# Performance work log

Measured on AMD Instinct MI355X. Metric: run time of the kernel, lower is better.

## Reference

```python
import jax, jax.numpy as jnp
import numpy as np

HIDDEN = 128
HEADS = 8
HEAD_DIM = HIDDEN // HEADS


def setup_inputs() -> dict:
    key = jax.random.key(0)
    ks = jax.random.split(key, 10)
    B, V = 2, 768
    s = 1.0 / np.sqrt(HIDDEN)
    return {
        "x": jax.random.normal(ks[0], (B, V, HIDDEN), dtype=jnp.float32),
        "edge_gate": jax.random.uniform(ks[1], (B, V, V, HIDDEN), dtype=jnp.float32),
        "Wq": jax.random.normal(ks[2], (HIDDEN, HIDDEN), dtype=jnp.float32) * s,
        "bq": jnp.zeros((HIDDEN,), dtype=jnp.float32),
        "Wk": jax.random.normal(ks[3], (HIDDEN, HIDDEN), dtype=jnp.float32) * s,
        "bk": jnp.zeros((HIDDEN,), dtype=jnp.float32),
        "Wv": jax.random.normal(ks[4], (HIDDEN, HIDDEN), dtype=jnp.float32) * s,
        "bv": jnp.zeros((HIDDEN,), dtype=jnp.float32),
        "Wo": jax.random.normal(ks[5], (HIDDEN, HIDDEN), dtype=jnp.float32) * s,
        "bo": jnp.zeros((HIDDEN,), dtype=jnp.float32),
    }


def reference(x, edge_gate, Wq, bq, Wk, bk, Wv, bv, Wo, bo):
    B, V, H = x.shape
    nh, hd = HEADS, HEAD_DIM
    # torch Linear: y = x @ W.T + b
    q = (x @ Wq.T + bq).reshape(B, V, nh, hd).transpose(0, 2, 1, 3)  # (B,nh,V,hd)
    k = (x @ Wk.T + bk).reshape(B, V, nh, hd).transpose(0, 2, 1, 3)
    v = (x @ Wv.T + bv).reshape(B, V, nh, hd).transpose(0, 2, 1, 3)
    scores = jnp.einsum("bhqd,bhkd->bhqk", q, k) / jnp.sqrt(jnp.float32(hd))
    edge_mask = jnp.mean(edge_gate, axis=-1)[:, None]  # (B,1,V,V)
    weights = jax.nn.softmax(scores * edge_mask, axis=-1)
    attended = jnp.einsum("bhqk,bhkd->bhqd", weights, v)
    attended = attended.transpose(0, 2, 1, 3).reshape(B, V, H)
    return attended @ Wo.T + bo
```

## Files before the change

kernel.cpp:

```cpp
#include <hip/hip_runtime.h>
#include <math.h>

#define BB 2
#define VV 768
#define HID 128
#define NH 8
#define HD 16

#define QKV_BLOCKS 768
#define EDGE_BLOCKS 2048
#define EDGE_WAVES (EDGE_BLOCKS * 4)
#define NPAIR (BB * VV * VV / 2)
#define EDGE_ITERS (NPAIR / EDGE_WAVES)

__global__ __launch_bounds__(256) void fused_qkv_edgemean(
    const float* __restrict__ x, const float* __restrict__ eg,
    const float* __restrict__ Wq, const float* __restrict__ bq,
    const float* __restrict__ Wk, const float* __restrict__ bk,
    const float* __restrict__ Wv, const float* __restrict__ bv,
    float* __restrict__ qh, float* __restrict__ kh, float* __restrict__ vh,
    float* __restrict__ mask) {
    __shared__ float xs[2][HID];
    if (blockIdx.x < QKV_BLOCKS) {
        const int half = threadIdx.x >> 7;
        const int c    = threadIdx.x & 127;
        const int row  = blockIdx.x * 2 + half;
        xs[half][c] = x[row * HID + c];
        __syncthreads();
        const float4* xs4 = (const float4*)xs[half];
        const float4* wq4 = (const float4*)(Wq + c * HID);
        const float4* wk4 = (const float4*)(Wk + c * HID);
        const float4* wv4 = (const float4*)(Wv + c * HID);
        float aq = 0.f, ak = 0.f, av = 0.f;
#pragma unroll
        for (int k4 = 0; k4 < HID / 4; ++k4) {
            float4 xv = xs4[k4];
            float4 a = wq4[k4];
            aq += xv.x * a.x + xv.y * a.y + xv.z * a.z + xv.w * a.w;
            float4 bv2 = wk4[k4];
            ak += xv.x * bv2.x + xv.y * bv2.y + xv.z * bv2.z + xv.w * bv2.w;
            float4 cv = wv4[k4];
            av += xv.x * cv.x + xv.y * cv.y + xv.z * cv.z + xv.w * cv.w;
        }
        const int b = row / VV, vi = row - b * VV;
        const int idx = ((b * NH + (c >> 4)) * VV + vi) * HD + (c & 15);
        qh[idx] = aq + bq[c];
        kh[idx] = ak + bk[c];
        vh[idx] = av + bv[c];
    } else {
        const int l = threadIdx.x & 63;
        const int w = (blockIdx.x - QKV_BLOCKS) * 4 + (threadIdx.x >> 6);
        const float4* eg4 = (const float4*)eg;
        const size_t wbase = (size_t)w * (EDGE_ITERS * 64);
#pragma unroll 4
        for (int it = 0; it < EDGE_ITERS; ++it) {
            float4 v = eg4[wbase + it * 64 + l];
            float s = (v.x + v.y) + (v.z + v.w);
            s += __shfl_xor(s, 1);
            s += __shfl_xor(s, 2);
            s += __shfl_xor(s, 4);
            s += __shfl_xor(s, 8);
            s += __shfl_xor(s, 16);
            if ((l & 31) == 0) {
                const int p = w * EDGE_ITERS + it;
                mask[p * 2 + (l >> 5)] = s * (1.0f / 128.0f);
            }
        }
    }
}

__global__ __launch_bounds__(256) void attn_kernel(
    const float* __restrict__ qh, const float* __restrict__ kh,
    const float* __restrict__ vh, const float* __restrict__ mask,
    float* __restrict__ att) {
    __shared__ float sc[4][2][VV];
    const int wid  = threadIdx.x >> 6;
    const int lane = threadIdx.x & 63;
    const int gw   = blockIdx.x * 4 + wid;
    const int pr   = gw % (VV / 2);
    const int bh   = gw / (VV / 2);
    const int b    = bh >> 3, h = bh & 7;
    const int q0i  = pr * 2, q1i = q0i + 1;

    const float4* qp0 = (const float4*)(qh + ((size_t)bh * VV + q0i) * HD);
    const float4 qa0 = qp0[0], qa1 = qp0[1], qa2 = qp0[2], qa3 = qp0[3];
    const float4* qp1 = (const float4*)(qh + ((size_t)bh * VV + q1i) * HD);
    const float4 qb0 = qp1[0], qb1 = qp1[1], qb2 = qp1[2], qb3 = qp1[3];

    const float* mrow0 = mask + ((size_t)b * VV + q0i) * VV;
    const float* mrow1 = mrow0 + VV;
    const float* kbase = kh + (size_t)bh * VV * HD;
    const float* vbase = vh + (size_t)bh * VV * HD;

    float m0 = -INFINITY, m1 = -INFINITY;
#pragma unroll
    for (int t = 0; t < VV / 64; ++t) {
        const int j = lane + 64 * t;
        const float4* kp = (const float4*)(kbase + j * HD);
        float4 k0 = kp[0], k1 = kp[1], k2 = kp[2], k3 = kp[3];
        float d0 = qa0.x * k0.x + qa0.y * k0.y + qa0.z * k0.z + qa0.w * k0.w
                 + qa1.x * k1.x + qa1.y * k1.y + qa1.z * k1.z + qa1.w * k1.w
                 + qa2.x * k2.x + qa2.y * k2.y + qa2.z * k2.z + qa2.w * k2.w
                 + qa3.x * k3.x + qa3.y * k3.y + qa3.z * k3.z + qa3.w * k3.w;
        float d1 = qb0.x * k0.x + qb0.y * k0.y + qb0.z * k0.z + qb0.w * k0.w
                 + qb1.x * k1.x + qb1.y * k1.y + qb1.z * k1.z + qb1.w * k1.w
                 + qb2.x * k2.x + qb2.y * k2.y + qb2.z * k2.z + qb2.w * k2.w
                 + qb3.x * k3.x + qb3.y * k3.y + qb3.z * k3.z + qb3.w * k3.w;
        float s0 = d0 * 0.25f * mrow0[j];
        float s1 = d1 * 0.25f * mrow1[j];
        sc[wid][0][j] = s0;
        sc[wid][1][j] = s1;
        m0 = fmaxf(m0, s0);
        m1 = fmaxf(m1, s1);
    }
#pragma unroll
    for (int off = 1; off < 64; off <<= 1) {
        m0 = fmaxf(m0, __shfl_xor(m0, off));
        m1 = fmaxf(m1, __shfl_xor(m1, off));
    }

    float sum0 = 0.f, sum1 = 0.f;
    float acc0[HD], acc1[HD];
#pragma unroll
    for (int d = 0; d < HD; ++d) { acc0[d] = 0.f; acc1[d] = 0.f; }
#pragma unroll
    for (int t = 0; t < VV / 64; ++t) {
        const int j = lane + 64 * t;
        float e0 = __expf(sc[wid][0][j] - m0);
        float e1 = __expf(sc[wid][1][j] - m1);
        sum0 += e0;
        sum1 += e1;
        const float4* vp = (const float4*)(vbase + j * HD);
        float4 v0 = vp[0], v1 = vp[1], v2 = vp[2], v3 = vp[3];
        acc0[0]  += e0 * v0.x; acc0[1]  += e0 * v0.y; acc0[2]  += e0 * v0.z; acc0[3]  += e0 * v0.w;
        acc0[4]  += e0 * v1.x; acc0[5]  += e0 * v1.y; acc0[6]  += e0 * v1.z; acc0[7]  += e0 * v1.w;
        acc0[8]  += e0 * v2.x; acc0[9]  += e0 * v2.y; acc0[10] += e0 * v2.z; acc0[11] += e0 * v2.w;
        acc0[12] += e0 * v3.x; acc0[13] += e0 * v3.y; acc0[14] += e0 * v3.z; acc0[15] += e0 * v3.w;
        acc1[0]  += e1 * v0.x; acc1[1]  += e1 * v0.y; acc1[2]  += e1 * v0.z; acc1[3]  += e1 * v0.w;
        acc1[4]  += e1 * v1.x; acc1[5]  += e1 * v1.y; acc1[6]  += e1 * v1.z; acc1[7]  += e1 * v1.w;
        acc1[8]  += e1 * v2.x; acc1[9]  += e1 * v2.y; acc1[10] += e1 * v2.z; acc1[11] += e1 * v2.w;
        acc1[12] += e1 * v3.x; acc1[13] += e1 * v3.y; acc1[14] += e1 * v3.z; acc1[15] += e1 * v3.w;
    }
#pragma unroll
    for (int off = 1; off < 64; off <<= 1) {
        sum0 += __shfl_xor(sum0, off);
        sum1 += __shfl_xor(sum1, off);
    }

#pragma unroll
    for (int i = 0; i < 8; ++i) {
        float sa = (lane & 1) ? acc0[i] : acc0[i + 8];
        float ra = __shfl_xor(sa, 1);
        acc0[i] = ((lane & 1) ? acc0[i + 8] : acc0[i]) + ra;
        float sb = (lane & 1) ? acc1[i] : acc1[i + 8];
        float rb = __shfl_xor(sb, 1);
        acc1[i] = ((lane & 1) ? acc1[i + 8] : acc1[i]) + rb;
    }
#pragma unroll
    for (int i = 0; i < 4; ++i) {
        float sa = (lane & 2) ? acc0[i] : acc0[i + 4];
        float ra = __shfl_xor(sa, 2);
        acc0[i] = ((lane & 2) ? acc0[i + 4] : acc0[i]) + ra;
        float sb = (lane & 2) ? acc1[i] : acc1[i + 4];
        float rb = __shfl_xor(sb, 2);
        acc1[i] = ((lane & 2) ? acc1[i + 4] : acc1[i]) + rb;
    }
#pragma unroll
    for (int i = 0; i < 2; ++i) {
        float sa = (lane & 4) ? acc0[i] : acc0[i + 2];
        float ra = __shfl_xor(sa, 4);
        acc0[i] = ((lane & 4) ? acc0[i + 2] : acc0[i]) + ra;
        float sb = (lane & 4) ? acc1[i] : acc1[i + 2];
        float rb = __shfl_xor(sb, 4);
        acc1[i] = ((lane & 4) ? acc1[i + 2] : acc1[i]) + rb;
    }
    {
        float sa = (lane & 8) ? acc0[0] : acc0[1];
        float ra = __shfl_xor(sa, 8);
        acc0[0] = ((lane & 8) ? acc0[1] : acc0[0]) + ra;
        float sb = (lane & 8) ? acc1[0] : acc1[1];
        float rb = __shfl_xor(sb, 8);
        acc1[0] = ((lane & 8) ? acc1[1] : acc1[0]) + rb;
    }
    acc0[0] += __shfl_xor(acc0[0], 16);
    acc0[0] += __shfl_xor(acc0[0], 32);
    acc1[0] += __shfl_xor(acc1[0], 16);
    acc1[0] += __shfl_xor(acc1[0], 32);

    const int d = ((lane & 1) << 3) | ((lane & 2) << 1) | ((lane & 4) >> 1) | ((lane & 8) >> 3);
    if (lane < HD) {
        att[((size_t)b * VV + q0i) * HID + h * HD + d] = acc0[0] / sum0;
        att[((size_t)b * VV + q1i) * HID + h * HD + d] = acc1[0] / sum1;
    }
}

__global__ __launch_bounds__(128) void outproj_kernel(
    const float* __restrict__ att, const float* __restrict__ Wo,
    const float* __restrict__ bo, float* __restrict__ out) {
    const int row = blockIdx.x;
    const int c   = threadIdx.x;
    __shared__ float xs[HID];
    xs[c] = att[row * HID + c];
    __syncthreads();
    const float4* xs4 = (const float4*)xs;
    const float4* wo4 = (const float4*)(Wo + c * HID);
    float a = 0.f;
#pragma unroll
    for (int k4 = 0; k4 < HID / 4; ++k4) {
        float4 xv = xs4[k4];
        float4 wv = wo4[k4];
        a += xv.x * wv.x + xv.y * wv.y + xv.z * wv.z + xv.w * wv.w;
    }
    out[row * HID + c] = a + bo[c];
}

extern "C" void kernel_launch(void* const* d_in, const int* in_sizes, int n_in,
                              void* d_out, int out_size, void* d_ws, size_t ws_size,
                              hipStream_t stream) {
    const float* x  = (const float*)d_in[0];
    const float* eg = (const float*)d_in[1];
    const float* Wq = (const float*)d_in[2];
    const float* bq = (const float*)d_in[3];
    const float* Wk = (const float*)d_in[4];
    const float* bk = (const float*)d_in[5];
    const float* Wv = (const float*)d_in[6];
    const float* bv = (const float*)d_in[7];
    const float* Wo = (const float*)d_in[8];
    const float* bo = (const float*)d_in[9];
    float* out = (float*)d_out;

    float* ws   = (float*)d_ws;
    float* mask = ws;
    float* qh   = mask + (size_t)BB * VV * VV;
    float* kh   = qh + (size_t)BB * VV * HID;
    float* vh   = kh + (size_t)BB * VV * HID;
    float* att  = vh + (size_t)BB * VV * HID;

    hipLaunchKernelGGL(fused_qkv_edgemean, dim3(QKV_BLOCKS + EDGE_BLOCKS), dim3(256), 0, stream,
                       x, eg, Wq, bq, Wk, bk, Wv, bv, qh, kh, vh, mask);
    hipLaunchKernelGGL(attn_kernel, dim3(BB * NH * VV / 8), dim3(256), 0, stream,
                       qh, kh, vh, mask, att);
    hipLaunchKernelGGL(outproj_kernel, dim3(BB * VV), dim3(128), 0, stream,
                       att, Wo, bo, out);
}
```

Baseline: 219.3 us.

## Reduce edge-gate rows per thread instead of wave-cooperative shuffle reduction

The edge-mean pass changes from wave-cooperative coalesced float4 loads with shuffle reductions to one thread per pair of rows. Each thread sums 256 contiguous floats in registers and writes one float2. The grid becomes one block per 512 rows, and edge blocks are placed ahead of the QKV blocks. This removes the shuffles and the strided scalar stores, but each load instruction now hits 64 addresses 1 KB apart, which risks poor coalescing and cache-line thrashing on the dominant 600 MB stream.

Result: slower. 227.4 us (+3.7%).

```diff
diff --git a/kernel.cpp b/kernel.cpp
--- a/kernel.cpp
+++ b/kernel.cpp
@@ -7,11 +7,9 @@
 #define NH 8
 #define HD 16
 
+#define NROWS (BB * VV * VV)
+#define EDGE_BLOCKS (NROWS / 2 / 256)
 #define QKV_BLOCKS 768
-#define EDGE_BLOCKS 2048
-#define EDGE_WAVES (EDGE_BLOCKS * 4)
-#define NPAIR (BB * VV * VV / 2)
-#define EDGE_ITERS (NPAIR / EDGE_WAVES)
 
 __global__ __launch_bounds__(256) void fused_qkv_edgemean(
     const float* __restrict__ x, const float* __restrict__ eg,
@@ -21,10 +19,32 @@
     float* __restrict__ qh, float* __restrict__ kh, float* __restrict__ vh,
     float* __restrict__ mask) {
     __shared__ float xs[2][HID];
-    if (blockIdx.x < QKV_BLOCKS) {
+    if (blockIdx.x < EDGE_BLOCKS) {
+        const int g = blockIdx.x * 256 + threadIdx.x;
+        const float4* p = (const float4*)eg + (size_t)g * 64;
+        float a0x = 0.f, a0y = 0.f, a0z = 0.f, a0w = 0.f;
+        float a1x = 0.f, a1y = 0.f, a1z = 0.f, a1w = 0.f;
+#pragma unroll
+        for (int kg = 0; kg < 8; ++kg) {
+#pragma unroll
+            for (int k4 = 0; k4 < 4; ++k4) {
+                float4 v = p[kg * 4 + k4];
+                a0x += v.x; a0y += v.y; a0z += v.z; a0w += v.w;
+            }
+#pragma unroll
+            for (int k4 = 0; k4 < 4; ++k4) {
+                float4 v = p[32 + kg * 4 + k4];
+                a1x += v.x; a1y += v.y; a1z += v.z; a1w += v.w;
+            }
+        }
+        float2 st;
+        st.x = ((a0x + a0y) + (a0z + a0w)) * (1.0f / 128.0f);
+        st.y = ((a1x + a1y) + (a1z + a1w)) * (1.0f / 128.0f);
+        ((float2*)mask)[g] = st;
+    } else {
         const int half = threadIdx.x >> 7;
         const int c    = threadIdx.x & 127;
-        const int row  = blockIdx.x * 2 + half;
+        const int row  = (blockIdx.x - EDGE_BLOCKS) * 2 + half;
         xs[half][c] = x[row * HID + c];
         __syncthreads();
         const float4* xs4 = (const float4*)xs[half];
@@ -47,25 +67,6 @@
         qh[idx] = aq + bq[c];
         kh[idx] = ak + bk[c];
         vh[idx] = av + bv[c];
-    } else {
-        const int l = threadIdx.x & 63;
-        const int w = (blockIdx.x - QKV_BLOCKS) * 4 + (threadIdx.x >> 6);
-        const float4* eg4 = (const float4*)eg;
-        const size_t wbase = (size_t)w * (EDGE_ITERS * 64);
-#pragma unroll 4
-        for (int it = 0; it < EDGE_ITERS; ++it) {
-            float4 v = eg4[wbase + it * 64 + l];
-            float s = (v.x + v.y) + (v.z + v.w);
-            s += __shfl_xor(s, 1);
-            s += __shfl_xor(s, 2);
-            s += __shfl_xor(s, 4);
-            s += __shfl_xor(s, 8);
-            s += __shfl_xor(s, 16);
-            if ((l & 31) == 0) {
-                const int p = w * EDGE_ITERS + it;
-                mask[p * 2 + (l >> 5)] = s * (1.0f / 128.0f);
-            }
-        }
     }
 }
 
@@ -236,7 +237,7 @@
     float* vh   = kh + (size_t)BB * VV * HID;
     float* att  = vh + (size_t)BB * VV * HID;
 
-    hipLaunchKernelGGL(fused_qkv_edgemean, dim3(QKV_BLOCKS + EDGE_BLOCKS), dim3(256), 0, stream,
+    hipLaunchKernelGGL(fused_qkv_edgemean, dim3(EDGE_BLOCKS + QKV_BLOCKS), dim3(256), 0, stream,
                        x, eg, Wq, bq, Wk, bk, Wv, bv, qh, kh, vh, mask);
     hipLaunchKernelGGL(attn_kernel, dim3(BB * NH * VV / 8), dim3(256), 0, stream,
                        qh, kh, vh, mask, att);
```

## Stream edge_gate through double-buffered LDS via async global-to-LDS loads

Applied to the files above, without the earlier changes.

Replaces the per-lane float4 edge-mean loop with a per-wave double-buffered pipeline that uses global_load_lds to stage 4KB chunks into shared memory while the previous chunk is reduced. The reduction becomes a transposed butterfly across lanes, producing eight row means per chunk with fewer shuffles per output. The goal is to keep more bytes in flight and hide memory latency on the bandwidth-bound pass. In exchange, the block now reserves 32KB of LDS, which may reduce occupancy, including for the QKV blocks.

Result: no change. 222.7 us (+1.5%).

```diff
diff --git a/kernel.cpp b/kernel.cpp
--- a/kernel.cpp
+++ b/kernel.cpp
@@ -10,8 +10,9 @@
 #define QKV_BLOCKS 768
 #define EDGE_BLOCKS 2048
 #define EDGE_WAVES (EDGE_BLOCKS * 4)
-#define NPAIR (BB * VV * VV / 2)
-#define EDGE_ITERS (NPAIR / EDGE_WAVES)
+#define CHUNKS_PER_WAVE 18
+#define LDS_AS(p) ((__attribute__((address_space(3))) void*)(p))
+#define GLB_AS(p) ((const __attribute__((address_space(1))) void*)(p))
 
 __global__ __launch_bounds__(256) void fused_qkv_edgemean(
     const float* __restrict__ x, const float* __restrict__ eg,
@@ -20,14 +21,15 @@
     const float* __restrict__ Wv, const float* __restrict__ bv,
     float* __restrict__ qh, float* __restrict__ kh, float* __restrict__ vh,
     float* __restrict__ mask) {
-    __shared__ float xs[2][HID];
+    __shared__ char smem[32768];
     if (blockIdx.x < QKV_BLOCKS) {
+        float* xs = (float*)smem;
         const int half = threadIdx.x >> 7;
         const int c    = threadIdx.x & 127;
         const int row  = blockIdx.x * 2 + half;
-        xs[half][c] = x[row * HID + c];
+        xs[half * HID + c] = x[row * HID + c];
         __syncthreads();
-        const float4* xs4 = (const float4*)xs[half];
+        const float4* xs4 = (const float4*)(xs + half * HID);
         const float4* wq4 = (const float4*)(Wq + c * HID);
         const float4* wk4 = (const float4*)(Wk + c * HID);
         const float4* wv4 = (const float4*)(Wv + c * HID);
@@ -48,22 +50,68 @@
         kh[idx] = ak + bk[c];
         vh[idx] = av + bv[c];
     } else {
-        const int l = threadIdx.x & 63;
-        const int w = (blockIdx.x - QKV_BLOCKS) * 4 + (threadIdx.x >> 6);
-        const float4* eg4 = (const float4*)eg;
-        const size_t wbase = (size_t)w * (EDGE_ITERS * 64);
-#pragma unroll 4
-        for (int it = 0; it < EDGE_ITERS; ++it) {
-            float4 v = eg4[wbase + it * 64 + l];
-            float s = (v.x + v.y) + (v.z + v.w);
-            s += __shfl_xor(s, 1);
-            s += __shfl_xor(s, 2);
-            s += __shfl_xor(s, 4);
-            s += __shfl_xor(s, 8);
-            s += __shfl_xor(s, 16);
-            if ((l & 31) == 0) {
-                const int p = w * EDGE_ITERS + it;
-                mask[p * 2 + (l >> 5)] = s * (1.0f / 128.0f);
+        const int l   = threadIdx.x & 63;
+        const int wid = threadIdx.x >> 6;
+        const int w   = (blockIdx.x - QKV_BLOCKS) * 4 + wid;
+        const char* gbase = (const char*)eg + (size_t)w * (CHUNKS_PER_WAVE * 4096);
+        char* lbase = smem + wid * 8192;
+
+#pragma unroll
+        for (int j = 0; j < 4; ++j)
+            __builtin_amdgcn_global_load_lds(GLB_AS(gbase + j * 1024 + l * 16),
+                                             LDS_AS(lbase + j * 1024), 16, 0, 0);
+#pragma unroll
+        for (int j = 0; j < 4; ++j)
+            __builtin_amdgcn_global_load_lds(GLB_AS(gbase + 4096 + j * 1024 + l * 16),
+                                             LDS_AS(lbase + 4096 + j * 1024), 16, 0, 0);
+
+#pragma unroll 1
+        for (int c = 0; c < CHUNKS_PER_WAVE; ++c) {
+            if (c == CHUNKS_PER_WAVE - 1)
+                asm volatile("s_waitcnt vmcnt(0)" ::: "memory");
+            else
+                asm volatile("s_waitcnt vmcnt(4)" ::: "memory");
+            __builtin_amdgcn_sched_barrier(0);
+
+            const float* bf = (const float*)(lbase + (c & 1) * 4096);
+            float A[16];
+#pragma unroll
+            for (int k = 0; k < 16; ++k) A[k] = bf[l + 64 * k];
+            float t[8];
+#pragma unroll
+            for (int r = 0; r < 8; ++r) t[r] = A[2 * r] + A[2 * r + 1];
+#pragma unroll
+            for (int i = 0; i < 4; ++i) {
+                float send = (l & 1) ? t[i] : t[i + 4];
+                float r = __shfl_xor(send, 1);
+                t[i] = ((l & 1) ? t[i + 4] : t[i]) + r;
+            }
+#pragma unroll
+            for (int i = 0; i < 2; ++i) {
+                float send = (l & 2) ? t[i] : t[i + 2];
+                float r = __shfl_xor(send, 2);
+                t[i] = ((l & 2) ? t[i + 2] : t[i]) + r;
+            }
+            {
+                float send = (l & 4) ? t[0] : t[1];
+                float r = __shfl_xor(send, 4);
+                t[0] = ((l & 4) ? t[1] : t[0]) + r;
+            }
+            t[0] += __shfl_xor(t[0], 8);
+            t[0] += __shfl_xor(t[0], 16);
+            t[0] += __shfl_xor(t[0], 32);
+            if (l < 8) {
+                const int d = ((l & 1) << 2) | (l & 2) | ((l & 4) >> 2);
+                mask[w * (CHUNKS_PER_WAVE * 8) + c * 8 + d] = t[0] * (1.0f / 128.0f);
+            }
+            if (c + 2 < CHUNKS_PER_WAVE) {
+                asm volatile("s_waitcnt lgkmcnt(0)" ::: "memory");
+                const char* gc = gbase + (size_t)(c + 2) * 4096;
+                char* lc = lbase + (c & 1) * 4096;
+#pragma unroll
+                for (int j = 0; j < 4; ++j)
+                    __builtin_amdgcn_global_load_lds(GLB_AS(gc + j * 1024 + l * 16),
+                                                     LDS_AS(lc + j * 1024), 16, 0, 0);
             }
         }
     }
```

## Pipeline edge-mask reduction chunks with attention and out-projection across launches

Applied to the files above, without the earlier changes.

Splits the edge_gate mean reduction into four quarter chunks. Each launch reduces one chunk while attention runs on query rows whose mask rows were finished by the previous launch. The last attention quarter is co-scheduled with the output projection of rows that are already complete, and a small tail kernel handles the remaining rows. The aim is to hide the bandwidth-bound edge_gate read behind attention compute instead of running the two back to back. In exchange it adds more kernel launches and boundaries between them, and it relies on a hard-coded chunk and row schedule.

Result: slower. 265.1 us (+20.9%).

```diff
diff --git a/kernel.cpp b/kernel.cpp
--- a/kernel.cpp
+++ b/kernel.cpp
@@ -7,13 +7,180 @@
 #define NH 8
 #define HD 16
 
+#define EQ_BLOCKS 512
 #define QKV_BLOCKS 768
-#define EDGE_BLOCKS 2048
-#define EDGE_WAVES (EDGE_BLOCKS * 4)
-#define NPAIR (BB * VV * VV / 2)
-#define EDGE_ITERS (NPAIR / EDGE_WAVES)
-
-__global__ __launch_bounds__(256) void fused_qkv_edgemean(
+#define ATT_BLOCKS 384
+#define PAIRS_PER_WAVE 72
+
+__device__ __forceinline__ void edge_wave(const float* __restrict__ eg,
+                                          float* __restrict__ mask,
+                                          int w, int l) {
+    const float4* eg4 = (const float4*)eg;
+    const size_t wbase = (size_t)w * (PAIRS_PER_WAVE * 64);
+#pragma unroll 4
+    for (int it = 0; it < PAIRS_PER_WAVE; ++it) {
+        float4 v = eg4[wbase + it * 64 + l];
+        float s = (v.x + v.y) + (v.z + v.w);
+        s += __shfl_xor(s, 1);
+        s += __shfl_xor(s, 2);
+        s += __shfl_xor(s, 4);
+        s += __shfl_xor(s, 8);
+        s += __shfl_xor(s, 16);
+        if ((l & 31) == 0) {
+            const int p = w * PAIRS_PER_WAVE + it;
+            mask[p * 2 + (l >> 5)] = s * (1.0f / 128.0f);
+        }
+    }
+}
+
+__device__ __forceinline__ void attn_wave(const float* __restrict__ qh,
+                                          const float* __restrict__ kh,
+                                          const float* __restrict__ vh,
+                                          const float* __restrict__ mask,
+                                          float* __restrict__ att,
+                                          float* sc,
+                                          int gw, int b, int vlo, int lane) {
+    const int h   = gw / 192;
+    const int prl = gw % 192;
+    const int bh  = b * NH + h;
+    const int q0i = vlo + 2 * prl, q1i = q0i + 1;
+
+    const float4* qp0 = (const float4*)(qh + ((size_t)bh * VV + q0i) * HD);
+    const float4 qa0 = qp0[0], qa1 = qp0[1], qa2 = qp0[2], qa3 = qp0[3];
+    const float4* qp1 = (const float4*)(qh + ((size_t)bh * VV + q1i) * HD);
+    const float4 qb0 = qp1[0], qb1 = qp1[1], qb2 = qp1[2], qb3 = qp1[3];
+
+    const float* mrow0 = mask + ((size_t)b * VV + q0i) * VV;
+    const float* mrow1 = mrow0 + VV;
+    const float* kbase = kh + (size_t)bh * VV * HD;
+    const float* vbase = vh + (size_t)bh * VV * HD;
+
+    float m0 = -INFINITY, m1 = -INFINITY;
+#pragma unroll
+    for (int t = 0; t < VV / 64; ++t) {
+        const int j = lane + 64 * t;
+        const float4* kp = (const float4*)(kbase + j * HD);
+        float4 k0 = kp[0], k1 = kp[1], k2 = kp[2], k3 = kp[3];
+        float d0 = qa0.x * k0.x + qa0.y * k0.y + qa0.z * k0.z + qa0.w * k0.w
+                 + qa1.x * k1.x + qa1.y * k1.y + qa1.z * k1.z + qa1.w * k1.w
+                 + qa2.x * k2.x + qa2.y * k2.y + qa2.z * k2.z + qa2.w * k2.w
+                 + qa3.x * k3.x + qa3.y * k3.y + qa3.z * k3.z + qa3.w * k3.w;
+        float d1 = qb0.x * k0.x + qb0.y * k0.y + qb0.z * k0.z + qb0.w * k0.w
+                 + qb1.x * k1.x + qb1.y * k1.y + qb1.z * k1.z + qb1.w * k1.w
+                 + qb2.x * k2.x + qb2.y * k2.y + qb2.z * k2.z + qb2.w * k2.w
+                 + qb3.x * k3.x + qb3.y * k3.y + qb3.z * k3.z + qb3.w * k3.w;
+        float s0 = d0 * 0.25f * mrow0[j];
+        float s1 = d1 * 0.25f * mrow1[j];
+        sc[j]      = s0;
+        sc[VV + j] = s1;
+        m0 = fmaxf(m0, s0);
+        m1 = fmaxf(m1, s1);
+    }
+#pragma unroll
+    for (int off = 1; off < 64; off <<= 1) {
+        m0 = fmaxf(m0, __shfl_xor(m0, off));
+        m1 = fmaxf(m1, __shfl_xor(m1, off));
+    }
+
+    float sum0 = 0.f, sum1 = 0.f;
+    float acc0[HD], acc1[HD];
+#pragma unroll
+    for (int d = 0; d < HD; ++d) { acc0[d] = 0.f; acc1[d] = 0.f; }
+#pragma unroll
+    for (int t = 0; t < VV / 64; ++t) {
+        const int j = lane + 64 * t;
+        float e0 = __expf(sc[j] - m0);
+        float e1 = __expf(sc[VV + j] - m1);
+        sum0 += e0;
+        sum1 += e1;
+        const float4* vp = (const float4*)(vbase + j * HD);
+        float4 v0 = vp[0], v1 = vp[1], v2 = vp[2], v3 = vp[3];
+        acc0[0]  += e0 * v0.x; acc0[1]  += e0 * v0.y; acc0[2]  += e0 * v0.z; acc0[3]  += e0 * v0.w;
+        acc0[4]  += e0 * v1.x; acc0[5]  += e0 * v1.y; acc0[6]  += e0 * v1.z; acc0[7]  += e0 * v1.w;
+        acc0[8]  += e0 * v2.x; acc0[9]  += e0 * v2.y; acc0[10] += e0 * v2.z; acc0[11] += e0 * v2.w;
+        acc0[12] += e0 * v3.x; acc0[13] += e0 * v3.y; acc0[14] += e0 * v3.z; acc0[15] += e0 * v3.w;
+        acc1[0]  += e1 * v0.x; acc1[1]  += e1 * v0.y; acc1[2]  += e1 * v0.z; acc1[3]  += e1 * v0.w;
+        acc1[4]  += e1 * v1.x; acc1[5]  += e1 * v1.y; acc1[6]  += e1 * v1.z; acc1[7]  += e1 * v1.w;
+        acc1[8]  += e1 * v2.x; acc1[9]  += e1 * v2.y; acc1[10] += e1 * v2.z; acc1[11] += e1 * v2.w;
+        acc1[12] += e1 * v3.x; acc1[13] += e1 * v3.y; acc1[14] += e1 * v3.z; acc1[15] += e1 * v3.w;
+    }
+#pragma unroll
+    for (int off = 1; off < 64; off <<= 1) {
+        sum0 += __shfl_xor(sum0, off);
+        sum1 += __shfl_xor(sum1, off);
+    }
+
+#pragma unroll
+    for (int i = 0; i < 8; ++i) {
+        float sa = (lane & 1) ? acc0[i] : acc0[i + 8];
+        float ra = __shfl_xor(sa, 1);
+        acc0[i] = ((lane & 1) ? acc0[i + 8] : acc0[i]) + ra;
+        float sb = (lane & 1) ? acc1[i] : acc1[i + 8];
+        float rb = __shfl_xor(sb, 1);
+        acc1[i] = ((lane & 1) ? acc1[i + 8] : acc1[i]) + rb;
+    }
+#pragma unroll
+    for (int i = 0; i < 4; ++i) {
+        float sa = (lane & 2) ? acc0[i] : acc0[i + 4];
+        float ra = __shfl_xor(sa, 2);
+        acc0[i] = ((lane & 2) ? acc0[i + 4] : acc0[i]) + ra;
+        float sb = (lane & 2) ? acc1[i] : acc1[i + 4];
+        float rb = __shfl_xor(sb, 2);
+        acc1[i] = ((lane & 2) ? acc1[i + 4] : acc1[i]) + rb;
+    }
+#pragma unroll
+    for (int i = 0; i < 2; ++i) {
+        float sa = (lane & 4) ? acc0[i] : acc0[i + 2];
+        float ra = __shfl_xor(sa, 4);
+        acc0[i] = ((lane & 4) ? acc0[i + 2] : acc0[i]) + ra;
+        float sb = (lane & 4) ? acc1[i] : acc1[i + 2];
+        float rb = __shfl_xor(sb, 4);
+        acc1[i] = ((lane & 4) ? acc1[i + 2] : acc1[i]) + rb;
+    }
+    {
+        float sa = (lane & 8) ? acc0[0] : acc0[1];
+        float ra = __shfl_xor(sa, 8);
+        acc0[0] = ((lane & 8) ? acc0[1] : acc0[0]) + ra;
+        float sb = (lane & 8) ? acc1[0] : acc1[1];
+        float rb = __shfl_xor(sb, 8);
+        acc1[0] = ((lane & 8) ? acc1[1] : acc1[0]) + rb;
+    }
+    acc0[0] += __shfl_xor(acc0[0], 16);
+    acc0[0] += __shfl_xor(acc0[0], 32);
+    acc1[0] += __shfl_xor(acc1[0], 16);
+    acc1[0] += __shfl_xor(acc1[0], 32);
+
+    const int d = ((lane & 1) << 3) | ((lane & 2) << 1) | ((lane & 4) >> 1) | ((lane & 8) >> 3);
+    if (lane < HD) {
+        att[((size_t)b * VV + q0i) * HID + h * HD + d] = acc0[0] / sum0;
+        att[((size_t)b * VV + q1i) * HID + h * HD + d] = acc1[0] / sum1;
+    }
+}
+
+__device__ __forceinline__ void outproj2_body(const float* __restrict__ att,
+                                              const float* __restrict__ Wo,
+                                              const float* __restrict__ bo,
+                                              float* __restrict__ out,
+                                              float* xs,
+                                              int row0) {
+    const int half = threadIdx.x >> 7;
+    const int c    = threadIdx.x & 127;
+    const int row  = row0 + half;
+    xs[half * HID + c] = att[(size_t)row * HID + c];
+    __syncthreads();
+    const float4* a4 = (const float4*)(xs + half * HID);
+    const float4* w4 = (const float4*)(Wo + c * HID);
+    float a = 0.f;
+#pragma unroll
+    for (int k4 = 0; k4 < HID / 4; ++k4) {
+        float4 xv = a4[k4];
+        float4 wv = w4[k4];
+        a += xv.x * wv.x + xv.y * wv.y + xv.z * wv.z + xv.w * wv.w;
+    }
+    out[(size_t)row * HID + c] = a + bo[c];
+}
+
+__global__ __launch_bounds__(256) void k_edge_qkv(
     const float* __restrict__ x, const float* __restrict__ eg,
     const float* __restrict__ Wq, const float* __restrict__ bq,
     const float* __restrict__ Wk, const float* __restrict__ bk,
@@ -21,10 +188,14 @@
     float* __restrict__ qh, float* __restrict__ kh, float* __restrict__ vh,
     float* __restrict__ mask) {
     __shared__ float xs[2][HID];
-    if (blockIdx.x < QKV_BLOCKS) {
+    const int lane = threadIdx.x & 63;
+    const int wid  = threadIdx.x >> 6;
+    if (blockIdx.x < EQ_BLOCKS) {
+        edge_wave(eg, mask, blockIdx.x * 4 + wid, lane);
+    } else {
         const int half = threadIdx.x >> 7;
         const int c    = threadIdx.x & 127;
-        const int row  = blockIdx.x * 2 + half;
+        const int row  = (blockIdx.x - EQ_BLOCKS) * 2 + half;
         xs[half][c] = x[row * HID + c];
         __syncthreads();
         const float4* xs4 = (const float4*)xs[half];
@@ -47,171 +218,47 @@
         qh[idx] = aq + bq[c];
         kh[idx] = ak + bk[c];
         vh[idx] = av + bv[c];
+    }
+}
+
+__global__ __launch_bounds__(256) void k_edge_attn(
+    const float* __restrict__ eg,
+    const float* __restrict__ qh, const float* __restrict__ kh,
+    const float* __restrict__ vh, float* __restrict__ mask,
+    float* __restrict__ att, int w_off, int ab, int avlo) {
+    __shared__ float sc[4][2][VV];
+    const int lane = threadIdx.x & 63;
+    const int wid  = threadIdx.x >> 6;
+    if (blockIdx.x < EQ_BLOCKS) {
+        edge_wave(eg, mask, w_off + blockIdx.x * 4 + wid, lane);
     } else {
-        const int l = threadIdx.x & 63;
-        const int w = (blockIdx.x - QKV_BLOCKS) * 4 + (threadIdx.x >> 6);
-        const float4* eg4 = (const float4*)eg;
-        const size_t wbase = (size_t)w * (EDGE_ITERS * 64);
-#pragma unroll 4
-        for (int it = 0; it < EDGE_ITERS; ++it) {
-            float4 v = eg4[wbase + it * 64 + l];
-            float s = (v.x + v.y) + (v.z + v.w);
-            s += __shfl_xor(s, 1);
-            s += __shfl_xor(s, 2);
-            s += __shfl_xor(s, 4);
-            s += __shfl_xor(s, 8);
-            s += __shfl_xor(s, 16);
-            if ((l & 31) == 0) {
-                const int p = w * EDGE_ITERS + it;
-                mask[p * 2 + (l >> 5)] = s * (1.0f / 128.0f);
-            }
-        }
-    }
-}
-
-__global__ __launch_bounds__(256) void attn_kernel(
+        const int gw = (blockIdx.x - EQ_BLOCKS) * 4 + wid;
+        attn_wave(qh, kh, vh, mask, att, &sc[wid][0][0], gw, ab, avlo, lane);
+    }
+}
+
+__global__ __launch_bounds__(256) void k_attn_outproj(
     const float* __restrict__ qh, const float* __restrict__ kh,
     const float* __restrict__ vh, const float* __restrict__ mask,
-    float* __restrict__ att) {
+    float* __restrict__ att,
+    const float* __restrict__ Wo, const float* __restrict__ bo,
+    float* __restrict__ out) {
     __shared__ float sc[4][2][VV];
+    const int lane = threadIdx.x & 63;
     const int wid  = threadIdx.x >> 6;
-    const int lane = threadIdx.x & 63;
-    const int gw   = blockIdx.x * 4 + wid;
-    const int pr   = gw % (VV / 2);
-    const int bh   = gw / (VV / 2);
-    const int b    = bh >> 3, h = bh & 7;
-    const int q0i  = pr * 2, q1i = q0i + 1;
-
-    const float4* qp0 = (const float4*)(qh + ((size_t)bh * VV + q0i) * HD);
-    const float4 qa0 = qp0[0], qa1 = qp0[1], qa2 = qp0[2], qa3 = qp0[3];
-    const float4* qp1 = (const float4*)(qh + ((size_t)bh * VV + q1i) * HD);
-    const float4 qb0 = qp1[0], qb1 = qp1[1], qb2 = qp1[2], qb3 = qp1[3];
-
-    const float* mrow0 = mask + ((size_t)b * VV + q0i) * VV;
-    const float* mrow1 = mrow0 + VV;
-    const float* kbase = kh + (size_t)bh * VV * HD;
-    const float* vbase = vh + (size_t)bh * VV * HD;
-
-    float m0 = -INFINITY, m1 = -INFINITY;
-#pragma unroll
-    for (int t = 0; t < VV / 64; ++t) {
-        const int j = lane + 64 * t;
-        const float4* kp = (const float4*)(kbase + j * HD);
-        float4 k0 = kp[0], k1 = kp[1], k2 = kp[2], k3 = kp[3];
-        float d0 = qa0.x * k0.x + qa0.y * k0.y + qa0.z * k0.z + qa0.w * k0.w
-                 + qa1.x * k1.x + qa1.y * k1.y + qa1.z * k1.z + qa1.w * k1.w
-                 + qa2.x * k2.x + qa2.y * k2.y + qa2.z * k2.z + qa2.w * k2.w
-                 + qa3.x * k3.x + qa3.y * k3.y + qa3.z * k3.z + qa3.w * k3.w;
-        float d1 = qb0.x * k0.x + qb0.y * k0.y + qb0.z * k0.z + qb0.w * k0.w
-                 + qb1.x * k1.x + qb1.y * k1.y + qb1.z * k1.z + qb1.w * k1.w
-                 + qb2.x * k2.x + qb2.y * k2.y + qb2.z * k2.z + qb2.w * k2.w
-                 + qb3.x * k3.x + qb3.y * k3.y + qb3.z * k3.z + qb3.w * k3.w;
-        float s0 = d0 * 0.25f * mrow0[j];
-        float s1 = d1 * 0.25f * mrow1[j];
-        sc[wid][0][j] = s0;
-        sc[wid][1][j] = s1;
-        m0 = fmaxf(m0, s0);
-        m1 = fmaxf(m1, s1);
-    }
-#pragma unroll
-    for (int off = 1; off < 64; off <<= 1) {
-        m0 = fmaxf(m0, __shfl_xor(m0, off));
-        m1 = fmaxf(m1, __shfl_xor(m1, off));
-    }
-
-    float sum0 = 0.f, sum1 = 0.f;
-    float acc0[HD], acc1[HD];
-#pragma unroll
-    for (int d = 0; d < HD; ++d) { acc0[d] = 0.f; acc1[d] = 0.f; }
-#pragma unroll
-    for (int t = 0; t < VV / 64; ++t) {
-        const int j = lane + 64 * t;
-        float e0 = __expf(sc[wid][0][j] - m0);
-        float e1 = __expf(sc[wid][1][j] - m1);
-        sum0 += e0;
-        sum1 += e1;
-        const float4* vp = (const float4*)(vbase + j * HD);
-        float4 v0 = vp[0], v1 = vp[1], v2 = vp[2], v3 = vp[3];
-        acc0[0]  += e0 * v0.x; acc0[1]  += e0 * v0.y; acc0[2]  += e0 * v0.z; acc0[3]  += e0 * v0.w;
-        acc0[4]  += e0 * v1.x; acc0[5]  += e0 * v1.y; acc0[6]  += e0 * v1.z; acc0[7]  += e0 * v1.w;
-        acc0[8]  += e0 * v2.x; acc0[9]  += e0 * v2.y; acc0[10] += e0 * v2.z; acc0[11] += e0 * v2.w;
-        acc0[12] += e0 * v3.x; acc0[13] += e0 * v3.y; acc0[14] += e0 * v3.z; acc0[15] += e0 * v3.w;
-        acc1[0]  += e1 * v0.x; acc1[1]  += e1 * v0.y; acc1[2]  += e1 * v0.z; acc1[3]  += e1 * v0.w;
-        acc1[4]  += e1 * v1.x; acc1[5]  += e1 * v1.y; acc1[6]  += e1 * v1.z; acc1[7]  += e1 * v1.w;
-        acc1[8]  += e1 * v2.x; acc1[9]  += e1 * v2.y; acc1[10] += e1 * v2.z; acc1[11] += e1 * v2.w;
-        acc1[12] += e1 * v3.x; acc1[13] += e1 * v3.y; acc1[14] += e1 * v3.z; acc1[15] += e1 * v3.w;
-    }
-#pragma unroll
-    for (int off = 1; off < 64; off <<= 1) {
-        sum0 += __shfl_xor(sum0, off);
-        sum1 += __shfl_xor(sum1, off);
-    }
-
-#pragma unroll
-    for (int i = 0; i < 8; ++i) {
-        float sa = (lane & 1) ? acc0[i] : acc0[i + 8];
-        float ra = __shfl_xor(sa, 1);
-        acc0[i] = ((lane & 1) ? acc0[i + 8] : acc0[i]) + ra;
-        float sb = (lane & 1) ? acc1[i] : acc1[i + 8];
-        float rb = __shfl_xor(sb, 1);
-        acc1[i] = ((lane & 1) ? acc1[i + 8] : acc1[i]) + rb;
-    }
-#pragma unroll
-    for (int i = 0; i < 4; ++i) {
-        float sa = (lane & 2) ? acc0[i] : acc0[i + 4];
-        float ra = __shfl_xor(sa, 2);
-        acc0[i] = ((lane & 2) ? acc0[i + 4] : acc0[i]) + ra;
-        float sb = (lane & 2) ? acc1[i] : acc1[i + 4];
-        float rb = __shfl_xor(sb, 2);
-        acc1[i] = ((lane & 2) ? acc1[i + 4] : acc1[i]) + rb;
-    }
-#pragma unroll
-    for (int i = 0; i < 2; ++i) {
-        float sa = (lane & 4) ? acc0[i] : acc0[i + 2];
-        float ra = __shfl_xor(sa, 4);
-        acc0[i] = ((lane & 4) ? acc0[i + 2] : acc0[i]) + ra;
-        float sb = (lane & 4) ? acc1[i] : acc1[i + 2];
-        float rb = __shfl_xor(sb, 4);
-        acc1[i] = ((lane & 4) ? acc1[i + 2] : acc1[i]) + rb;
-    }
-    {
-        float sa = (lane & 8) ? acc0[0] : acc0[1];
-        float ra = __shfl_xor(sa, 8);
-        acc0[0] = ((lane & 8) ? acc0[1] : acc0[0]) + ra;
-        float sb = (lane & 8) ? acc1[0] : acc1[1];
-        float rb = __shfl_xor(sb, 8);
-        acc1[0] = ((lane & 8) ? acc1[1] : acc1[0]) + rb;
-    }
-    acc0[0] += __shfl_xor(acc0[0], 16);
-    acc0[0] += __shfl_xor(acc0[0], 32);
-    acc1[0] += __shfl_xor(acc1[0], 16);
-    acc1[0] += __shfl_xor(acc1[0], 32);
-
-    const int d = ((lane & 1) << 3) | ((lane & 2) << 1) | ((lane & 4) >> 1) | ((lane & 8) >> 3);
-    if (lane < HD) {
-        att[((size_t)b * VV + q0i) * HID + h * HD + d] = acc0[0] / sum0;
-        att[((size_t)b * VV + q1i) * HID + h * HD + d] = acc1[0] / sum1;
-    }
-}
-
-__global__ __launch_bounds__(128) void outproj_kernel(
+    if (blockIdx.x < ATT_BLOCKS) {
+        const int gw = blockIdx.x * 4 + wid;
+        attn_wave(qh, kh, vh, mask, att, &sc[wid][0][0], gw, 1, 384, lane);
+    } else {
+        outproj2_body(att, Wo, bo, out, &sc[0][0][0], (blockIdx.x - ATT_BLOCKS) * 2);
+    }
+}
+
+__global__ __launch_bounds__(256) void k_outproj_tail(
     const float* __restrict__ att, const float* __restrict__ Wo,
     const float* __restrict__ bo, float* __restrict__ out) {
-    const int row = blockIdx.x;
-    const int c   = threadIdx.x;
-    __shared__ float xs[HID];
-    xs[c] = att[row * HID + c];
-    __syncthreads();
-    const float4* xs4 = (const float4*)xs;
-    const float4* wo4 = (const float4*)(Wo + c * HID);
-    float a = 0.f;
-#pragma unroll
-    for (int k4 = 0; k4 < HID / 4; ++k4) {
-        float4 xv = xs4[k4];
-        float4 wv = wo4[k4];
-        a += xv.x * wv.x + xv.y * wv.y + xv.z * wv.z + xv.w * wv.w;
-    }
-    out[row * HID + c] = a + bo[c];
+    __shared__ float xs[2][HID];
+    outproj2_body(att, Wo, bo, out, &xs[0][0], 1152 + blockIdx.x * 2);
 }
 
 extern "C" void kernel_launch(void* const* d_in, const int* in_sizes, int n_in,
@@ -236,10 +283,16 @@
     float* vh   = kh + (size_t)BB * VV * HID;
     float* att  = vh + (size_t)BB * VV * HID;
 
-    hipLaunchKernelGGL(fused_qkv_edgemean, dim3(QKV_BLOCKS + EDGE_BLOCKS), dim3(256), 0, stream,
+    hipLaunchKernelGGL(k_edge_qkv, dim3(EQ_BLOCKS + QKV_BLOCKS), dim3(256), 0, stream,
                        x, eg, Wq, bq, Wk, bk, Wv, bv, qh, kh, vh, mask);
-    hipLaunchKernelGGL(attn_kernel, dim3(BB * NH * VV / 8), dim3(256), 0, stream,
-                       qh, kh, vh, mask, att);
-    hipLaunchKernelGGL(outproj_kernel, dim3(BB * VV), dim3(128), 0, stream,
+    hipLaunchKernelGGL(k_edge_attn, dim3(EQ_BLOCKS + ATT_BLOCKS), dim3(256), 0, stream,
+                       eg, qh, kh, vh, mask, att, 2048, 0, 0);
+    hipLaunchKernelGGL(k_edge_attn, dim3(EQ_BLOCKS + ATT_BLOCKS), dim3(256), 0, stream,
+                       eg, qh, kh, vh, mask, att, 4096, 0, 384);
+    hipLaunchKernelGGL(k_edge_attn, dim3(EQ_BLOCKS + ATT_BLOCKS), dim3(256), 0, stream,
+                       eg, qh, kh, vh, mask, att, 6144, 1, 0);
+    hipLaunchKernelGGL(k_attn_outproj, dim3(ATT_BLOCKS + 576), dim3(256), 0, stream,
+                       qh, kh, vh, mask, att, Wo, bo, out);
+    hipLaunchKernelGGL(k_outproj_tail, dim3(192), dim3(256), 0, stream,
                        att, Wo, bo, out);
 }
```
